# Kernel tuning notes

Hardware: AMD Instinct MI355X
Metric: run time of the kernel (lower is better)

## Reference

```python
import jax, jax.numpy as jnp
import numpy as np

B, N, L, H, D, IN = 512, 128, 10, 16, 8, 16
NT = B * N
E = NT * 16

def _lin(key, fan_in, shape):
    b = 1.0 / np.sqrt(fan_in)
    return jax.random.uniform(key, shape, jnp.float32, -b, b)

def setup_inputs() -> dict:
    key = jax.random.key(0)
    ks = jax.random.split(key, 12)
    x = jax.random.normal(ks[0], (NT, IN), jnp.float32)
    # within-graph random edges so to_dense_adj is well defined
    g = jax.random.randint(ks[1], (E,), 0, B)
    i = jax.random.randint(ks[2], (E,), 0, N)
    j = jax.random.randint(ks[3], (E,), 0, N)
    edge_index = jnp.stack([g * N + i, g * N + j]).astype(jnp.int32)
    return dict(
        x=x,
        gin_w1=_lin(ks[4], H, (2, L, H, H)),   # [ld/ud, layer, H, H]
        gin_b1=_lin(ks[5], H, (2, L, H)),
        gin_w2=_lin(ks[6], H, (2, L, H, H)),
        gin_b2=_lin(ks[7], H, (2, L, H)),
        mean_w=_lin(ks[8], H, (2, H, D)),
        mean_b=jnp.zeros((2, D), jnp.float32),
        std_w=_lin(ks[9], H, (2, H, D)),
        std_b=jnp.zeros((2, D), jnp.float32),
        edge_index=edge_index,
    )

def _encoder(x, w1, b1, w2, b2, mw, mb, sw, sb, src, dst):
    # PyG GIN stack: GINConv(MLP[Lin->ReLU->Lin]), eps=0, sum aggregation,
    # ReLU between layers (dropout = identity in eval mode).
    h = x
    for l in range(L):
        agg = jax.ops.segment_sum(h[src], dst, num_segments=NT)
        t = h + agg  # (1+eps)*x + sum_{j in N(i)} x_j with eps=0
        t = jnp.maximum(t @ w1[l] + b1[l], 0.0) @ w2[l] + b2[l]
        h = jnp.maximum(t, 0.0) if l < L - 1 else t
    mean = h @ mw + mb
    std = jax.nn.softplus(h @ sw + sb)
    return mean, std

def reference(x, gin_w1, gin_b1, gin_w2, gin_b2, mean_w, mean_b, std_w, std_b, edge_index):
    src, dst = edge_index[0], edge_index[1]
    enc = jax.vmap(_encoder, in_axes=(None, 0, 0, 0, 0, 0, 0, 0, 0, None, None))
    mean, std = enc(x, gin_w1, gin_b1, gin_w2, gin_b2,
                    mean_w, mean_b, std_w, std_b, src, dst)  # [2, NT, D]
    # reparameterized sample: eps ~ N(0,1) (prior.sample, detached)
    eps = jax.random.normal(jax.random.key(42), (2, NT, D), jnp.float32)
    z = mean + std * eps
    z_ld = z[0].reshape(B, N, D)
    z_ud = z[1].reshape(B, N, D)
    logits = jnp.einsum('bnd,bmd->bnm', z_ld, z_ud)  # per-graph inner-product decode
    dense_adj = jnp.zeros((B, N, N), jnp.float32).at[src // N, src % N, dst % N].add(1.0)
    n_pos = dense_adj.sum()
    posw = (B * N * N - n_pos) / n_pos
    # BCE-with-logits, pos_weight, reduction='sum'
    nll = jnp.sum(posw * dense_adj * jax.nn.softplus(-logits)
                  + (1.0 - dense_adj) * jax.nn.softplus(logits))
    # KL(N(mean,std) || N(0,1)), summed over both encoders
    kl = jnp.sum(-jnp.log(std) + 0.5 * (std * std + mean * mean) - 0.5)
    return nll, kl, jax.nn.sigmoid(logits), dense_adj
```

## Files before the change

### kernel.cpp

```cpp
#include <hip/hip_runtime.h>

#define B_    512
#define N_    128
#define L_    10
#define H_    16
#define D_    8
#define NT_   65536
#define E_    1048576
#define NNB_  8388608
#define CAP_  4096
#define CCAP_ 2816
#define HS_   20

__device__ __forceinline__ unsigned rotl32(unsigned v, int r){ return (v<<r)|(v>>(32-r)); }

__device__ __forceinline__ void threefry2x32(unsigned c0, unsigned c1, unsigned &o0, unsigned &o1){
  const unsigned ks0 = 0u, ks1 = 42u, ks2 = 0u ^ 42u ^ 0x1BD11BDAu;
  unsigned x0 = c0 + ks0, x1 = c1 + ks1;
#define TFR(r) { x0 += x1; x1 = rotl32(x1, r); x1 ^= x0; }
  TFR(13) TFR(15) TFR(26) TFR(6)   x0 += ks1; x1 += ks2 + 1u;
  TFR(17) TFR(29) TFR(16) TFR(24)  x0 += ks2; x1 += ks0 + 2u;
  TFR(13) TFR(15) TFR(26) TFR(6)   x0 += ks0; x1 += ks1 + 3u;
  TFR(17) TFR(29) TFR(16) TFR(24)  x0 += ks1; x1 += ks2 + 4u;
  TFR(13) TFR(15) TFR(26) TFR(6)   x0 += ks2; x1 += ks0 + 5u;
#undef TFR
  o0 = x0; o1 = x1;
}

__device__ __forceinline__ float erfinv_f(float x){
  float w = -log1pf(-x*x);
  float p;
  if (w < 5.0f) {
    w -= 2.5f;
    p = 2.81022636e-08f;
    p = fmaf(p, w, 3.43273939e-07f);
    p = fmaf(p, w, -3.5233877e-06f);
    p = fmaf(p, w, -4.39150654e-06f);
    p = fmaf(p, w, 0.00021858087f);
    p = fmaf(p, w, -0.00125372503f);
    p = fmaf(p, w, -0.00417768164f);
    p = fmaf(p, w, 0.246640727f);
    p = fmaf(p, w, 1.50140941f);
  } else {
    w = sqrtf(w) - 3.0f;
    p = -0.000200214257f;
    p = fmaf(p, w, 0.000100950558f);
    p = fmaf(p, w, 0.00134934322f);
    p = fmaf(p, w, -0.00367342844f);
    p = fmaf(p, w, 0.00573950773f);
    p = fmaf(p, w, -0.0076224613f);
    p = fmaf(p, w, 0.00943887047f);
    p = fmaf(p, w, 1.00167406f);
    p = fmaf(p, w, 2.83297682f);
  }
  return p * x;
}

__device__ __forceinline__ float softplus_f(float x){
  return fmaxf(x, 0.0f) + log1pf(expf(-fabsf(x)));
}

__device__ __forceinline__ void blockReduceAdd(double v, double* target){
  __shared__ double red[4];
  int lane = threadIdx.x & 63;
  int w    = threadIdx.x >> 6;
  #pragma unroll
  for(int off = 32; off > 0; off >>= 1) v += __shfl_down(v, off);
  if(lane == 0) red[w] = v;
  __syncthreads();
  if(threadIdx.x == 0){
    double s = red[0];
    int nw = (blockDim.x + 63) >> 6;
    for(int k = 1; k < nw; k++) s += red[k];
    atomicAdd(target, s);
  }
}

__global__ __launch_bounds__(256)
void k_bin(const int* __restrict__ ei, int* __restrict__ gcount,
           unsigned short* __restrict__ ebuf){
  __shared__ int cnt[512];
  __shared__ int gb[512];
  const int t = threadIdx.x;
  cnt[t] = 0; cnt[t + 256] = 0;
  __syncthreads();
  int kv[8];
  const int base = blockIdx.x * 2048;
  #pragma unroll
  for(int q = 0; q < 8; q++){
    int e = base + q*256 + t;
    int s = ei[e];
    int d = ei[E_ + e];
    int g = d >> 7;
    kv[q] = (g << 14) | ((s & 127) << 7) | (d & 127);
    atomicAdd(&cnt[g], 1);
  }
  __syncthreads();
  #pragma unroll
  for(int g = 0; g < 512; g += 256){
    int c = cnt[g + t];
    gb[g + t] = c ? atomicAdd(&gcount[g + t], c) : 0;
    cnt[g + t] = 0;
  }
  __syncthreads();
  #pragma unroll
  for(int q = 0; q < 8; q++){
    int g = kv[q] >> 14;
    int pos = atomicAdd(&cnt[g], 1);
    int idx = gb[g] + pos;
    if(idx < CAP_) ebuf[(size_t)g*CAP_ + idx] = (unsigned short)(kv[q] & 0x3FFF);
  }
}

__global__ __launch_bounds__(128)
void k_csr(const unsigned short* __restrict__ ebuf, const int* __restrict__ gcount,
           unsigned short* __restrict__ gcol, int* __restrict__ grow){
  __shared__ int cnt[128], off[128], sc[128];
  const int b = blockIdx.x, t = threadIdx.x;
  int ec = gcount[b]; if(ec > CAP_) ec = CAP_;
  const unsigned short* eb = ebuf + (size_t)b*CAP_;
  cnt[t] = 0;
  __syncthreads();
  for(int q = t; q < ec; q += 128) atomicAdd(&cnt[eb[q] & 127], 1);
  __syncthreads();
  int pdeg = (cnt[t] + 3) & ~3;
  sc[t] = pdeg;
  __syncthreads();
  for(int o = 1; o < 128; o <<= 1){
    int v = (t >= o) ? sc[t - o] : 0;
    __syncthreads();
    sc[t] += v;
    __syncthreads();
  }
  off[t] = sc[t] - pdeg;
  grow[b*129 + t] = off[t];
  if(t == 127) grow[b*129 + 128] = sc[127];
  cnt[t] = 0;
  __syncthreads();
  {
    uint4 s128; s128.x = s128.y = s128.z = s128.w = 0x00800080u;
    uint4* g4 = (uint4*)(gcol + (size_t)b*CCAP_);
    #pragma unroll
    for(int k = 0; k < 3; k++){ int q = t + 128*k; if(q < CCAP_/8) g4[q] = s128; }
  }
  __syncthreads();
  for(int q = t; q < ec; q += 128){
    int pk = eb[q];
    int d = pk & 127;
    int pos = atomicAdd(&cnt[d], 1);
    int idx = off[d] + pos;
    if(idx < CCAP_) gcol[(size_t)b*CCAP_ + idx] = (unsigned short)(pk >> 7);
  }
}

__global__ __launch_bounds__(256, 4)
void k_mega(const float* __restrict__ x, const unsigned short* __restrict__ gcol,
            const int* __restrict__ grow,
            const float* __restrict__ gw1, const float* __restrict__ gb1,
            const float* __restrict__ gw2, const float* __restrict__ gb2,
            const float* __restrict__ mw,  const float* __restrict__ mb,
            const float* __restrict__ sw,  const float* __restrict__ sb,
            float* __restrict__ z, double* acc){
  __shared__ __align__(16) float hh[2][129*HS_ + 4];
  __shared__ __align__(16) unsigned short col_l[CCAP_];
  const int b = blockIdx.x, e = blockIdx.y, t = threadIdx.x;
  const int i = t >> 1, p = t & 1;

  {
    const float4* x4 = (const float4*)x + (size_t)b*512;
    #pragma unroll
    for(int k = 0; k < 2; k++){
      int q = t + 256*k;
      float4 v = x4[q];
      *(float4*)&hh[0][(q >> 2)*HS_ + (q & 3)*4] = v;
    }
    if(t < 16){ hh[0][128*HS_ + t] = 0.0f; hh[1][128*HS_ + t] = 0.0f; }
  }
  {
    const uint4* gc4 = (const uint4*)(gcol + (size_t)b*CCAP_);
    uint4* cl4 = (uint4*)col_l;
    #pragma unroll
    for(int k = 0; k < 2; k++){ int q = t + 256*k; if(q < CCAP_/8) cl4[q] = gc4[q]; }
  }
  const int r0 = grow[b*129 + i], r1 = grow[b*129 + i + 1];
  __syncthreads();

  const float* w1g = gw1 + e*(L_*256);
  const float* w2g = gw2 + e*(L_*256);
  const float* b1g = gb1 + e*(L_*16);
  const float* b2g = gb2 + e*(L_*16);

  for(int l = 0; l < L_; l++){
    const float* hb = hh[l & 1];
    float*       hn = hh[(l + 1) & 1];
    float a[8];
    {
      const float4* hp = (const float4*)&hb[i*HS_ + p*8];
      float4 s0 = hp[0], s1 = hp[1];
      a[0]=s0.x; a[1]=s0.y; a[2]=s0.z; a[3]=s0.w;
      a[4]=s1.x; a[5]=s1.y; a[6]=s1.z; a[7]=s1.w;
    }
    for(int r = r0; r < r1; r += 4){
      ushort4 c4 = *(const ushort4*)&col_l[r];
      const float4* n0 = (const float4*)&hb[c4.x*HS_ + p*8];
      const float4* n1 = (const float4*)&hb[c4.y*HS_ + p*8];
      const float4* n2 = (const float4*)&hb[c4.z*HS_ + p*8];
      const float4* n3 = (const float4*)&hb[c4.w*HS_ + p*8];
      #pragma unroll
      for(int c = 0; c < 2; c++){
        float4 v0 = n0[c], v1 = n1[c], v2 = n2[c], v3 = n3[c];
        a[c*4+0] += v0.x + v1.x + v2.x + v3.x;
        a[c*4+1] += v0.y + v1.y + v2.y + v3.y;
        a[c*4+2] += v0.z + v1.z + v2.z + v3.z;
        a[c*4+3] += v0.w + v1.w + v2.w + v3.w;
      }
    }
    float ag[16];
    #pragma unroll
    for(int q = 0; q < 8; q++){
      float o = __shfl_xor(a[q], 1);
      ag[q]     = p ? o    : a[q];
      ag[q + 8] = p ? a[q] : o;
    }
    float u[16];
    #pragma unroll
    for(int j = 0; j < 16; j++){
      float s = b1g[l*16 + j];
      #pragma unroll
      for(int k = 0; k < 16; k++) s = fmaf(ag[k], w1g[l*256 + k*16 + j], s);
      u[j] = fmaxf(s, 0.0f);
    }
    float ov[16];
    #pragma unroll
    for(int c = 0; c < 16; c++){
      float s = b2g[l*16 + c];
      #pragma unroll
      for(int k = 0; k < 16; k++) s = fmaf(u[k], w2g[l*256 + k*16 + c], s);
      ov[c] = (l < L_-1) ? fmaxf(s, 0.0f) : s;
    }
    {
      float4* hw = (float4*)&hn[i*HS_ + p*8];
      hw[0] = make_float4(p ? ov[8]  : ov[0], p ? ov[9]  : ov[1],
                          p ? ov[10] : ov[2], p ? ov[11] : ov[3]);
      hw[1] = make_float4(p ? ov[12] : ov[4], p ? ov[13] : ov[5],
                          p ? ov[14] : ov[6], p ? ov[15] : ov[7]);
    }
    __syncthreads();
  }

  float hv[16];
  {
    const float4* hp = (const float4*)&hh[0][i*HS_];
    float4 a0 = hp[0], a1 = hp[1], a2 = hp[2], a3 = hp[3];
    hv[0]=a0.x; hv[1]=a0.y; hv[2]=a0.z; hv[3]=a0.w;
    hv[4]=a1.x; hv[5]=a1.y; hv[6]=a1.z; hv[7]=a1.w;
    hv[8]=a2.x; hv[9]=a2.y; hv[10]=a2.z; hv[11]=a2.w;
    hv[12]=a3.x; hv[13]=a3.y; hv[14]=a3.z; hv[15]=a3.w;
  }
  const float* mwg = mw + e*128; const float* mbg = mb + e*8;
  const float* swg = sw + e*128; const float* sbg = sb + e*8;
  float md[8], sd[8];
  #pragma unroll
  for(int d = 0; d < 8; d++){
    float mm = mbg[d], ss = sbg[d];
    #pragma unroll
    for(int k = 0; k < 16; k++){
      mm = fmaf(hv[k], mwg[k*8 + d], mm);
      ss = fmaf(hv[k], swg[k*8 + d], ss);
    }
    md[d] = mm; sd[d] = ss;
  }
  double kll = 0.0;
  float zv[4];
  unsigned fbase = ((unsigned)e*NT_ + (unsigned)(b*128 + i))*8u + (unsigned)(p*4);
  #pragma unroll
  for(int dd = 0; dd < 4; dd++){
    float mm = p ? md[4+dd] : md[dd];
    float ss = p ? sd[4+dd] : sd[dd];
    float stdv = softplus_f(ss);
    unsigned o0, o1; threefry2x32(0u, fbase + dd, o0, o1);
    unsigned bits = o0 ^ o1;
    float uu = __uint_as_float((bits >> 9) | 0x3f800000u) - 1.0f;
    const float lo = -0.99999994f;
    float uval = fmaxf(lo, fmaf(uu, 2.0f, lo));
    float eps = 1.41421356f * erfinv_f(uval);
    zv[dd] = mm + stdv * eps;
    float stdc = fmaxf(stdv, 1e-37f);
    float term = 0.5f*(stdv*stdv + mm*mm) - logf(stdc) - 0.5f;
    if(!(term == term) || term > 1e30f) term = 1e30f;
    kll += (double)term;
  }
  {
    float4* zp = (float4*)(z + (size_t)fbase);
    zp[0] = make_float4(zv[0], zv[1], zv[2], zv[3]);
  }
  blockReduceAdd(kll, acc + 1);
}

#define TSB_ 132
__global__ __launch_bounds__(256, 4)
void k_decode(const float* __restrict__ z, const unsigned short* __restrict__ ebuf,
              const int* __restrict__ gcount, float* __restrict__ sig,
              float* __restrict__ adj, double* acc){
  __shared__ float zl[512];
  __shared__ unsigned tile32[64*TSB_/4];
  const int b = blockIdx.x >> 1, h = blockIdx.x & 1, t = threadIdx.x;
  const int col = t & 127, rg = t >> 7;
  const float* zld = z + (size_t)b*1024 + h*512;
  #pragma unroll
  for(int k = 0; k < 2; k++) zl[t + 256*k] = zld[t + 256*k];
  {
    uint4 zz; zz.x = zz.y = zz.z = zz.w = 0u;
    uint4* t4 = (uint4*)tile32;
    for(int k = t; k < 64*TSB_/16; k += 256) t4[k] = zz;
  }
  float zb[8];
  {
    const float4* zu4 = (const float4*)(z + (size_t)NT_*8 + (size_t)b*1024 + col*8);
    float4 u0 = zu4[0], u1 = zu4[1];
    zb[0]=u0.x; zb[1]=u0.y; zb[2]=u0.z; zb[3]=u0.w;
    zb[4]=u1.x; zb[5]=u1.y; zb[6]=u1.z; zb[7]=u1.w;
  }
  __syncthreads();
  {
    int ec = gcount[b]; if(ec > CAP_) ec = CAP_;
    const unsigned short* eb = ebuf + (size_t)b*CAP_;
    for(int q = t; q < ec; q += 256){
      int pk = eb[q];
      int src = pk >> 7;
      if((src >> 6) == h){
        int cell = (src & 63)*TSB_ + (pk & 127);
        atomicAdd(&tile32[cell >> 2], 1u << ((cell & 3)*8));
      }
    }
  }
  __syncthreads();
  double local = 0.0;
  float* sigb = sig + (size_t)b*16384 + h*8192;
  float* adjb = adj + (size_t)b*16384 + h*8192;
  for(int r = 0; r < 32; r++){
    int n = rg*32 + r;
    float4 a0 = *(const float4*)&zl[n*8];
    float4 a1 = *(const float4*)&zl[n*8 + 4];
    float xx = a0.x*zb[0] + a0.y*zb[1] + a0.z*zb[2] + a0.w*zb[3]
             + a1.x*zb[4] + a1.y*zb[5] + a1.z*zb[6] + a1.w*zb[7];
    unsigned packed = tile32[(n*TSB_ + col) >> 2];
    float ad = (float)((packed >> ((col & 3)*8)) & 0xFF);
    float sg = 1.0f / (1.0f + expf(-xx));
    float cc  = log1pf(expf(-fabsf(xx)));
    float spp = fmaxf(xx, 0.0f) + cc;
    float spn = fmaxf(-xx, 0.0f) + cc;
    local += (double)(7.0f*ad*spn + (1.0f - ad)*spp);
    sigb[n*128 + col] = sg;
    adjb[n*128 + col] = ad;
  }
  blockReduceAdd(local, acc + 0);
}

__device__ __forceinline__ float clamp_finite(double v){
  if(v != v) return 0.0f;
  if(v >  3.3e38) return  3.3e38f;
  if(v < -3.3e38) return -3.3e38f;
  return (float)v;
}
__global__ void k_final(const double* __restrict__ acc, float* __restrict__ out){
  if(threadIdx.x == 0){
    out[0] = clamp_finite(acc[0]);
    out[1] = clamp_finite(acc[1]);
  }
}

extern "C" void kernel_launch(void* const* d_in, const int* in_sizes, int n_in,
                              void* d_out, int out_size, void* d_ws, size_t ws_size,
                              hipStream_t stream){
  const float* x   = (const float*)d_in[0];
  const float* gw1 = (const float*)d_in[1];
  const float* gb1 = (const float*)d_in[2];
  const float* gw2 = (const float*)d_in[3];
  const float* gb2 = (const float*)d_in[4];
  const float* mw  = (const float*)d_in[5];
  const float* mb  = (const float*)d_in[6];
  const float* sw  = (const float*)d_in[7];
  const float* sb  = (const float*)d_in[8];
  const int*   ei  = (const int*)d_in[9];

  float* out = (float*)d_out;
  float* sig = out + 2;
  float* adj = out + 2 + NNB_;

  char* ws = (char*)d_ws;
  int*            gcount = (int*)(ws);
  double*         acc    = (double*)(ws + 2048);
  unsigned short* ebuf   = (unsigned short*)(ws + 4096);
  unsigned short* gcol   = (unsigned short*)(ws + 4096 + 2*512*CAP_);
  int*            grow   = (int*)(ws + 4096 + 2*512*CAP_ + 2*512*CCAP_);
  float*          z      = (float*)(ws + 4096 + 2*512*CAP_ + 2*512*CCAP_ + 4*512*132);

  hipMemsetAsync(ws, 0, 4096, stream);

  k_bin   <<<E_/2048, 256, 0, stream>>>(ei, gcount, ebuf);
  k_csr   <<<B_, 128, 0, stream>>>(ebuf, gcount, gcol, grow);
  k_mega  <<<dim3(B_, 2), 256, 0, stream>>>(x, gcol, grow, gw1, gb1, gw2, gb2,
                                            mw, mb, sw, sb, z, acc);
  k_decode<<<B_*2, 256, 0, stream>>>(z, ebuf, gcount, sig, adj, acc);
  k_final <<<1, 64, 0, stream>>>(acc, out);
}
```

Baseline: 250.7 us.

## Replace atomic edge binning with count/prefix/place passes and fuse final reduction

Edge binning is split into three passes: per-block counts per graph, a per-graph warp-scan prefix over blocks, and a placement pass. This replaces the global atomicAdd slot reservation with deterministic offsets. The memset and the k_final launch are removed by zeroing the accumulators in k_prefix and having the last k_decode block write the outputs via a done counter. In exchange the edge list is read twice and there are two extra kernel launches and about 2 MB of count/offset traffic.

```diff
diff --git a/kernel.cpp b/kernel.cpp
--- a/kernel.cpp
+++ b/kernel.cpp
@@ -11,6 +11,7 @@
 #define CAP_  4096
 #define CCAP_ 2816
 #define HS_   20
+#define NBLK_ 512
 
 __device__ __forceinline__ unsigned rotl32(unsigned v, int r){ return (v<<r)|(v>>(32-r)); }
 
@@ -77,14 +78,57 @@
 }
 
 __global__ __launch_bounds__(256)
-void k_bin(const int* __restrict__ ei, int* __restrict__ gcount,
-           unsigned short* __restrict__ ebuf){
+void k_count(const int* __restrict__ ei, int* __restrict__ gcnt){
   __shared__ int cnt[512];
-  __shared__ int gb[512];
   const int t = threadIdx.x;
   cnt[t] = 0; cnt[t + 256] = 0;
   __syncthreads();
-  int kv[8];
+  const int base = blockIdx.x * 2048;
+  #pragma unroll
+  for(int q = 0; q < 8; q++){
+    int d = ei[E_ + base + q*256 + t];
+    atomicAdd(&cnt[d >> 7], 1);
+  }
+  __syncthreads();
+  gcnt[blockIdx.x*512 + t]       = cnt[t];
+  gcnt[blockIdx.x*512 + t + 256] = cnt[t + 256];
+}
+
+__global__ __launch_bounds__(64)
+void k_prefix(const int* __restrict__ gcnt, int* __restrict__ goff,
+              int* __restrict__ gcount, double* acc, int* done){
+  const int g = blockIdx.x, lane = threadIdx.x;
+  if(g == 0 && lane < 4){
+    if(lane < 2) acc[lane] = 0.0;
+    if(lane == 2) *done = 0;
+  }
+  int base = 0;
+  for(int r = 0; r < 8; r++){
+    int blk = r*64 + lane;
+    int v = gcnt[blk*512 + g];
+    int pre = v;
+    #pragma unroll
+    for(int o = 1; o < 64; o <<= 1){
+      int u = __shfl_up(pre, o);
+      if(lane >= o) pre += u;
+    }
+    int excl = pre - v;
+    goff[blk*512 + g] = base + excl;
+    base += __shfl(pre, 63);
+  }
+  if(lane == 0) gcount[g] = base;
+}
+
+__global__ __launch_bounds__(256)
+void k_place(const int* __restrict__ ei, const int* __restrict__ goff,
+             unsigned short* __restrict__ ebuf){
+  __shared__ int pos[512];
+  __shared__ int off_l[512];
+  const int t = threadIdx.x;
+  pos[t] = 0; pos[t + 256] = 0;
+  off_l[t]       = goff[blockIdx.x*512 + t];
+  off_l[t + 256] = goff[blockIdx.x*512 + t + 256];
+  __syncthreads();
   const int base = blockIdx.x * 2048;
   #pragma unroll
   for(int q = 0; q < 8; q++){
@@ -92,23 +136,9 @@
     int s = ei[e];
     int d = ei[E_ + e];
     int g = d >> 7;
-    kv[q] = (g << 14) | ((s & 127) << 7) | (d & 127);
-    atomicAdd(&cnt[g], 1);
-  }
-  __syncthreads();
-  #pragma unroll
-  for(int g = 0; g < 512; g += 256){
-    int c = cnt[g + t];
-    gb[g + t] = c ? atomicAdd(&gcount[g + t], c) : 0;
-    cnt[g + t] = 0;
-  }
-  __syncthreads();
-  #pragma unroll
-  for(int q = 0; q < 8; q++){
-    int g = kv[q] >> 14;
-    int pos = atomicAdd(&cnt[g], 1);
-    int idx = gb[g] + pos;
-    if(idx < CAP_) ebuf[(size_t)g*CAP_ + idx] = (unsigned short)(kv[q] & 0x3FFF);
+    int p = atomicAdd(&pos[g], 1);
+    int idx = off_l[g] + p;
+    if(idx < CAP_) ebuf[(size_t)g*CAP_ + idx] = (unsigned short)(((s & 127) << 7) | (d & 127));
   }
 }
 
@@ -298,10 +328,16 @@
 }
 
 #define TSB_ 132
+__device__ __forceinline__ float clamp_finite(double v){
+  if(v != v) return 0.0f;
+  if(v >  3.3e38) return  3.3e38f;
+  if(v < -3.3e38) return -3.3e38f;
+  return (float)v;
+}
 __global__ __launch_bounds__(256, 4)
 void k_decode(const float* __restrict__ z, const unsigned short* __restrict__ ebuf,
               const int* __restrict__ gcount, float* __restrict__ sig,
-              float* __restrict__ adj, double* acc){
+              float* __restrict__ adj, double* acc, int* done, float* out){
   __shared__ float zl[512];
   __shared__ unsigned tile32[64*TSB_/4];
   const int b = blockIdx.x >> 1, h = blockIdx.x & 1, t = threadIdx.x;
@@ -355,18 +391,14 @@
     adjb[n*128 + col] = ad;
   }
   blockReduceAdd(local, acc + 0);
-}
-
-__device__ __forceinline__ float clamp_finite(double v){
-  if(v != v) return 0.0f;
-  if(v >  3.3e38) return  3.3e38f;
-  if(v < -3.3e38) return -3.3e38f;
-  return (float)v;
-}
-__global__ void k_final(const double* __restrict__ acc, float* __restrict__ out){
   if(threadIdx.x == 0){
-    out[0] = clamp_finite(acc[0]);
-    out[1] = clamp_finite(acc[1]);
+    __threadfence();
+    if(atomicAdd(done, 1) == 2*B_ - 1){
+      double nll = atomicAdd(acc + 0, 0.0);
+      double kl  = atomicAdd(acc + 1, 0.0);
+      out[0] = clamp_finite(nll);
+      out[1] = clamp_finite(kl);
+    }
   }
 }
 
@@ -389,19 +421,22 @@
   float* adj = out + 2 + NNB_;
 
   char* ws = (char*)d_ws;
-  int*            gcount = (int*)(ws);
-  double*         acc    = (double*)(ws + 2048);
-  unsigned short* ebuf   = (unsigned short*)(ws + 4096);
-  unsigned short* gcol   = (unsigned short*)(ws + 4096 + 2*512*CAP_);
-  int*            grow   = (int*)(ws + 4096 + 2*512*CAP_ + 2*512*CCAP_);
-  float*          z      = (float*)(ws + 4096 + 2*512*CAP_ + 2*512*CCAP_ + 4*512*132);
-
-  hipMemsetAsync(ws, 0, 4096, stream);
-
-  k_bin   <<<E_/2048, 256, 0, stream>>>(ei, gcount, ebuf);
+  size_t o = 0;
+  int*            gcount = (int*)(ws + o);        o += 512*4;
+  double*         acc    = (double*)(ws + o);     o += 2*8;
+  int*            done   = (int*)(ws + o);        o += 4;  o = (o+255)&~255ULL;
+  int*            gcnt   = (int*)(ws + o);        o += (size_t)NBLK_*512*4;
+  int*            goff   = (int*)(ws + o);        o += (size_t)NBLK_*512*4;
+  unsigned short* ebuf   = (unsigned short*)(ws + o); o += (size_t)512*CAP_*2;
+  unsigned short* gcol   = (unsigned short*)(ws + o); o += (size_t)512*CCAP_*2;
+  int*            grow   = (int*)(ws + o);        o += (size_t)512*129*4;
+  float*          z      = (float*)(ws + o);      o += (size_t)2*NT_*8*4;
+
+  k_count <<<NBLK_, 256, 0, stream>>>(ei, gcnt);
+  k_prefix<<<512, 64, 0, stream>>>(gcnt, goff, gcount, acc, done);
+  k_place <<<NBLK_, 256, 0, stream>>>(ei, goff, ebuf);
   k_csr   <<<B_, 128, 0, stream>>>(ebuf, gcount, gcol, grow);
   k_mega  <<<dim3(B_, 2), 256, 0, stream>>>(x, gcol, grow, gw1, gb1, gw2, gb2,
                                             mw, mb, sw, sb, z, acc);
-  k_decode<<<B_*2, 256, 0, stream>>>(z, ebuf, gcount, sig, adj, acc);
-  k_final <<<1, 64, 0, stream>>>(acc, out);
-}
+  k_decode<<<B_*2, 256, 0, stream>>>(z, ebuf, gcount, sig, adj, acc, done, out);
+}
```

Measured after the change: 279.5 us. +11.5%, slower.

## Use odd shared-memory row stride and fold final reduction into decode kernel

Applied to the files above, without the earlier changes.

Changes the per-node row stride of the shared hidden-state buffer from 20 to 17 floats. An odd stride spreads the random neighbor gathers across LDS banks and cuts bank conflicts, but it forces scalar LDS loads and stores in place of float4 accesses. It also drops the separate k_final launch: the last k_decode block, found with an atomic done-counter, writes the two scalar losses. The workspace layout is recomputed so the counter sits inside the memset region.

```diff
diff --git a/kernel.cpp b/kernel.cpp
--- a/kernel.cpp
+++ b/kernel.cpp
@@ -10,7 +10,7 @@
 #define NNB_  8388608
 #define CAP_  4096
 #define CCAP_ 2816
-#define HS_   20
+#define HS_   17
 
 __device__ __forceinline__ unsigned rotl32(unsigned v, int r){ return (v<<r)|(v>>(32-r)); }
 
@@ -161,7 +161,7 @@
             const float* __restrict__ mw,  const float* __restrict__ mb,
             const float* __restrict__ sw,  const float* __restrict__ sb,
             float* __restrict__ z, double* acc){
-  __shared__ __align__(16) float hh[2][129*HS_ + 4];
+  __shared__ float hh[2][129*HS_ + 1];
   __shared__ __align__(16) unsigned short col_l[CCAP_];
   const int b = blockIdx.x, e = blockIdx.y, t = threadIdx.x;
   const int i = t >> 1, p = t & 1;
@@ -172,7 +172,8 @@
     for(int k = 0; k < 2; k++){
       int q = t + 256*k;
       float4 v = x4[q];
-      *(float4*)&hh[0][(q >> 2)*HS_ + (q & 3)*4] = v;
+      float* dst = &hh[0][(q >> 2)*HS_ + (q & 3)*4];
+      dst[0] = v.x; dst[1] = v.y; dst[2] = v.z; dst[3] = v.w;
     }
     if(t < 16){ hh[0][128*HS_ + t] = 0.0f; hh[1][128*HS_ + t] = 0.0f; }
   }
@@ -195,24 +196,19 @@
     float*       hn = hh[(l + 1) & 1];
     float a[8];
     {
-      const float4* hp = (const float4*)&hb[i*HS_ + p*8];
-      float4 s0 = hp[0], s1 = hp[1];
-      a[0]=s0.x; a[1]=s0.y; a[2]=s0.z; a[3]=s0.w;
-      a[4]=s1.x; a[5]=s1.y; a[6]=s1.z; a[7]=s1.w;
+      const float* sp = &hb[i*HS_ + p*8];
+      #pragma unroll
+      for(int k = 0; k < 8; k++) a[k] = sp[k];
     }
     for(int r = r0; r < r1; r += 4){
       ushort4 c4 = *(const ushort4*)&col_l[r];
-      const float4* n0 = (const float4*)&hb[c4.x*HS_ + p*8];
-      const float4* n1 = (const float4*)&hb[c4.y*HS_ + p*8];
-      const float4* n2 = (const float4*)&hb[c4.z*HS_ + p*8];
-      const float4* n3 = (const float4*)&hb[c4.w*HS_ + p*8];
+      const float* n0 = &hb[c4.x*HS_ + p*8];
+      const float* n1 = &hb[c4.y*HS_ + p*8];
+      const float* n2 = &hb[c4.z*HS_ + p*8];
+      const float* n3 = &hb[c4.w*HS_ + p*8];
       #pragma unroll
-      for(int c = 0; c < 2; c++){
-        float4 v0 = n0[c], v1 = n1[c], v2 = n2[c], v3 = n3[c];
-        a[c*4+0] += v0.x + v1.x + v2.x + v3.x;
-        a[c*4+1] += v0.y + v1.y + v2.y + v3.y;
-        a[c*4+2] += v0.z + v1.z + v2.z + v3.z;
-        a[c*4+3] += v0.w + v1.w + v2.w + v3.w;
+      for(int k = 0; k < 8; k++){
+        a[k] += n0[k] + n1[k] + n2[k] + n3[k];
       }
     }
     float ag[16];
@@ -239,23 +235,18 @@
       ov[c] = (l < L_-1) ? fmaxf(s, 0.0f) : s;
     }
     {
-      float4* hw = (float4*)&hn[i*HS_ + p*8];
-      hw[0] = make_float4(p ? ov[8]  : ov[0], p ? ov[9]  : ov[1],
-                          p ? ov[10] : ov[2], p ? ov[11] : ov[3]);
-      hw[1] = make_float4(p ? ov[12] : ov[4], p ? ov[13] : ov[5],
-                          p ? ov[14] : ov[6], p ? ov[15] : ov[7]);
+      float* hw = &hn[i*HS_ + p*8];
+      #pragma unroll
+      for(int k = 0; k < 8; k++) hw[k] = p ? ov[8 + k] : ov[k];
     }
     __syncthreads();
   }
 
   float hv[16];
   {
-    const float4* hp = (const float4*)&hh[0][i*HS_];
-    float4 a0 = hp[0], a1 = hp[1], a2 = hp[2], a3 = hp[3];
-    hv[0]=a0.x; hv[1]=a0.y; hv[2]=a0.z; hv[3]=a0.w;
-    hv[4]=a1.x; hv[5]=a1.y; hv[6]=a1.z; hv[7]=a1.w;
-    hv[8]=a2.x; hv[9]=a2.y; hv[10]=a2.z; hv[11]=a2.w;
-    hv[12]=a3.x; hv[13]=a3.y; hv[14]=a3.z; hv[15]=a3.w;
+    const float* hp = &hh[0][i*HS_];
+    #pragma unroll
+    for(int k = 0; k < 16; k++) hv[k] = hp[k];
   }
   const float* mwg = mw + e*128; const float* mbg = mb + e*8;
   const float* swg = sw + e*128; const float* sbg = sb + e*8;
@@ -298,10 +289,16 @@
 }
 
 #define TSB_ 132
+__device__ __forceinline__ float clamp_finite(double v){
+  if(v != v) return 0.0f;
+  if(v >  3.3e38) return  3.3e38f;
+  if(v < -3.3e38) return -3.3e38f;
+  return (float)v;
+}
 __global__ __launch_bounds__(256, 4)
 void k_decode(const float* __restrict__ z, const unsigned short* __restrict__ ebuf,
               const int* __restrict__ gcount, float* __restrict__ sig,
-              float* __restrict__ adj, double* acc){
+              float* __restrict__ adj, double* acc, int* done, float* out){
   __shared__ float zl[512];
   __shared__ unsigned tile32[64*TSB_/4];
   const int b = blockIdx.x >> 1, h = blockIdx.x & 1, t = threadIdx.x;
@@ -355,18 +352,14 @@
     adjb[n*128 + col] = ad;
   }
   blockReduceAdd(local, acc + 0);
-}
-
-__device__ __forceinline__ float clamp_finite(double v){
-  if(v != v) return 0.0f;
-  if(v >  3.3e38) return  3.3e38f;
-  if(v < -3.3e38) return -3.3e38f;
-  return (float)v;
-}
-__global__ void k_final(const double* __restrict__ acc, float* __restrict__ out){
   if(threadIdx.x == 0){
-    out[0] = clamp_finite(acc[0]);
-    out[1] = clamp_finite(acc[1]);
+    __threadfence();
+    if(atomicAdd(done, 1) == 2*B_ - 1){
+      double nll = atomicAdd(acc + 0, 0.0);
+      double kl  = atomicAdd(acc + 1, 0.0);
+      out[0] = clamp_finite(nll);
+      out[1] = clamp_finite(kl);
+    }
   }
 }
 
@@ -389,12 +382,14 @@
   float* adj = out + 2 + NNB_;
 
   char* ws = (char*)d_ws;
-  int*            gcount = (int*)(ws);
-  double*         acc    = (double*)(ws + 2048);
-  unsigned short* ebuf   = (unsigned short*)(ws + 4096);
-  unsigned short* gcol   = (unsigned short*)(ws + 4096 + 2*512*CAP_);
-  int*            grow   = (int*)(ws + 4096 + 2*512*CAP_ + 2*512*CCAP_);
-  float*          z      = (float*)(ws + 4096 + 2*512*CAP_ + 2*512*CCAP_ + 4*512*132);
+  size_t o = 0;
+  int*            gcount = (int*)(ws + o);        o += 512*4;
+  double*         acc    = (double*)(ws + o);     o += 2*8;
+  int*            done   = (int*)(ws + o);        o += 4;  o = (o+255)&~255ULL;
+  unsigned short* ebuf   = (unsigned short*)(ws + o); o += (size_t)512*CAP_*2;
+  unsigned short* gcol   = (unsigned short*)(ws + o); o += (size_t)512*CCAP_*2;
+  int*            grow   = (int*)(ws + o);        o += (size_t)512*129*4;
+  float*          z      = (float*)(ws + o);      o += (size_t)2*NT_*8*4;
 
   hipMemsetAsync(ws, 0, 4096, stream);
 
@@ -402,6 +397,5 @@
   k_csr   <<<B_, 128, 0, stream>>>(ebuf, gcount, gcol, grow);
   k_mega  <<<dim3(B_, 2), 256, 0, stream>>>(x, gcol, grow, gw1, gb1, gw2, gb2,
                                             mw, mb, sw, sb, z, acc);
-  k_decode<<<B_*2, 256, 0, stream>>>(z, ebuf, gcount, sig, adj, acc);
-  k_final <<<1, 64, 0, stream>>>(acc, out);
-}
+  k_decode<<<B_*2, 256, 0, stream>>>(z, ebuf, gcount, sig, adj, acc, done, out);
+}
```

Result: slower. 309.5 us (+23.5%).
